# Performance work log

Measured on AMD Instinct MI355X. Metric: run time of the kernel, lower is better.

## Reference

```python
import jax, jax.numpy as jnp
import numpy as np

B, NQ, NKV = 4, 2048, 2048
D_MODEL, N_HEADS, D_K = 1024, 16, 64


def setup_inputs() -> dict:
    key = jax.random.key(0)
    ks = jax.random.split(key, 7)
    s = 1.0 / np.sqrt(D_MODEL)
    return {
        "x": jax.random.normal(ks[0], (B, NQ, D_MODEL), jnp.float32),
        "encoding": jax.random.normal(ks[1], (B, NKV, D_MODEL), jnp.float32),
        "position_bias": jax.random.normal(ks[2], (1, N_HEADS, NQ, NKV), jnp.float32),
        "Wq": jax.random.normal(ks[3], (D_MODEL, D_MODEL), jnp.float32) * s,
        "Wk": jax.random.normal(ks[4], (D_MODEL, D_MODEL), jnp.float32) * s,
        "Wv": jax.random.normal(ks[5], (D_MODEL, D_MODEL), jnp.float32) * s,
        "Wo": jax.random.normal(ks[6], (D_MODEL, D_MODEL), jnp.float32) * s,
    }


def _split_heads(t):
    b, n, _ = t.shape
    return t.reshape(b, n, N_HEADS, D_K).transpose(0, 2, 1, 3)


def reference(x, encoding, position_bias, Wq, Wk, Wv, Wo):
    # Projections (flax Dense, no bias): y = x @ kernel
    Q = _split_heads(x @ Wq)            # [B,H,NQ,Dk]
    K = _split_heads(encoding @ Wk)     # [B,H,NKV,Dk]
    V = _split_heads(encoding @ Wv)     # [B,H,NKV,Dk]
    # T5-style: NO 1/sqrt(d_k) scaling; additive position bias before softmax
    scores = jnp.einsum('bhqd,bhkd->bhqk', Q, K) + position_bias
    attn = jax.nn.softmax(scores, axis=-1)
    ctx = jnp.einsum('bhqk,bhkd->bhqd', attn, V)    # [B,H,NQ,Dk]
    ctx = ctx.transpose(0, 2, 1, 3).reshape(x.shape[0], x.shape[1], D_MODEL)
    return ctx @ Wo
```

## Files before the change

kernel.cpp:

```cpp
#include <hip/hip_runtime.h>

#define B_   4
#define NQ_  2048
#define NKV_ 2048
#define H_   16
#define DK_  64
#define DM_  1024
#define DKV_ 2048

typedef _Float16 f16x8 __attribute__((ext_vector_type(8)));
typedef _Float16 f16x4 __attribute__((ext_vector_type(4)));
typedef float    f32x4 __attribute__((ext_vector_type(4)));

__device__ __forceinline__ void gload_lds16(const void* g, void* l) {
  __builtin_amdgcn_global_load_lds(
      (const __attribute__((address_space(1))) unsigned int*)g,
      (__attribute__((address_space(3))) unsigned int*)l, 16, 0, 0);
}

__global__ __launch_bounds__(256) void cast_f16(const float* __restrict__ in,
                                                _Float16* __restrict__ out, int n4) {
  int i = blockIdx.x * 256 + threadIdx.x;
  if (i >= n4) return;
  float4 v = ((const float4*)in)[i];
  f16x4 o = {(_Float16)v.x, (_Float16)v.y, (_Float16)v.z, (_Float16)v.w};
  *(f16x4*)(out + (size_t)i * 4) = o;
}

__global__ __launch_bounds__(256) void wtrans(const float* __restrict__ W,
                                              _Float16* __restrict__ Wt) {
  __shared__ float tile[32][33];
  int bx = blockIdx.x & 31, by = blockIdx.x >> 5;
  int tx = threadIdx.x & 31, ty = threadIdx.x >> 5;
#pragma unroll
  for (int j = 0; j < 4; ++j)
    tile[ty + j * 8][tx] = W[(size_t)(by * 32 + ty + j * 8) * 1024 + bx * 32 + tx];
  __syncthreads();
#pragma unroll
  for (int j = 0; j < 4; ++j)
    Wt[(size_t)(bx * 32 + ty + j * 8) * 1024 + by * 32 + tx] = (_Float16)tile[tx][ty + j * 8];
}

template <int F32OUT>
__global__ __launch_bounds__(256, 2) void gemm_bt(const _Float16* __restrict__ A,
                                                  const _Float16* __restrict__ Bt,
                                                  void* __restrict__ Cp,
                                                  int M, int N, int K) {
  __shared__ _Float16 As[128 * 32];
  __shared__ _Float16 Bs[128 * 32];
  const int nbn = N >> 7;
  const int bm = blockIdx.x / nbn, bn = blockIdx.x % nbn;
  const int t = threadIdx.x, w = t >> 6, l = t & 63;
  const int lr = l & 15, lg = l >> 4;
  const int wr = w >> 1, wc = w & 1;
  const int m0 = bm << 7, n0 = bn << 7;

  f32x4 acc[4][4] = {};

  for (int k0 = 0; k0 < K; k0 += 32) {
#pragma unroll
    for (int p = 0; p < 2; ++p) {
      int off = p * 4096 + w * 1024 + l * 16;
      int row = off >> 6;
      int col = (off & 63) >> 1;
      gload_lds16(A  + (size_t)(m0 + row) * K + k0 + col, (char*)As + p * 4096 + w * 1024);
      gload_lds16(Bt + (size_t)(n0 + row) * K + k0 + col, (char*)Bs + p * 4096 + w * 1024);
    }
    __syncthreads();
    f16x8 af[4], bq[4];
#pragma unroll
    for (int i = 0; i < 4; ++i) {
      af[i] = *(const f16x8*)((const char*)As + (wr * 64 + i * 16 + lr) * 64 + lg * 16);
      bq[i] = *(const f16x8*)((const char*)Bs + (wc * 64 + i * 16 + lr) * 64 + lg * 16);
    }
#pragma unroll
    for (int i = 0; i < 4; ++i)
#pragma unroll
      for (int j = 0; j < 4; ++j)
        acc[i][j] = __builtin_amdgcn_mfma_f32_16x16x32_f16(af[i], bq[j], acc[i][j], 0, 0, 0);
    __syncthreads();
  }
#pragma unroll
  for (int i = 0; i < 4; ++i)
#pragma unroll
    for (int j = 0; j < 4; ++j)
#pragma unroll
      for (int r = 0; r < 4; ++r) {
        size_t row = m0 + wr * 64 + i * 16 + lg * 4 + r;
        size_t col = n0 + wc * 64 + j * 16 + lr;
        if (F32OUT) ((float*)Cp)[row * N + col] = acc[i][j][r];
        else ((_Float16*)Cp)[row * N + col] = (_Float16)acc[i][j][r];
      }
}

__global__ __launch_bounds__(256) void vtrans(const _Float16* __restrict__ KVb,
                                              _Float16* __restrict__ Vt) {
  __shared__ _Float16 tile[64][72];
  int idx = blockIdx.x;
  int kt = idx & 31, h = (idx >> 5) & 15, b = idx >> 9;
  int kv0 = kt << 6;
  int t = threadIdx.x;
#pragma unroll
  for (int p = 0; p < 2; ++p) {
    int c = t + p * 256;
    int row = c >> 3, cb = (c & 7) * 16;
    f16x8 v = *(const f16x8*)(KVb + (size_t)(b * NKV_ + kv0 + row) * DKV_ + 1024 + h * 64 + cb / 2);
    *(f16x8*)((char*)&tile[row][0] + cb) = v;
  }
  __syncthreads();
  int d = t & 63, j0 = (t >> 6) * 2;
#pragma unroll
  for (int jj = 0; jj < 2; ++jj) {
    int kvs = (j0 + jj) * 8;
    f16x8 o;
#pragma unroll
    for (int u = 0; u < 8; ++u) o[u] = tile[kvs + u][d];
    *(f16x8*)(Vt + ((size_t)((b * H_ + h) * 64 + d)) * NKV_ + kv0 + kvs) = o;
  }
}

__global__ __launch_bounds__(256, 2) void attn(const _Float16* __restrict__ Qb,
                                               const _Float16* __restrict__ KVb,
                                               const _Float16* __restrict__ Vt,
                                               const float* __restrict__ bias,
                                               _Float16* __restrict__ ctx) {
  __shared__ _Float16 Ks[64 * 64];
  __shared__ _Float16 Vs[64 * 64];
  __shared__ _Float16 Ps[4][16 * 64];
  int idx = blockIdx.x;
  int b = idx & 3, qt = (idx >> 2) & 31, h = idx >> 7;
  int t = threadIdx.x, w = t >> 6, l = t & 63, lr = l & 15, lg = l >> 4;
  int qw = (qt << 6) + (w << 4);

  const _Float16* qp = Qb + (size_t)(b * NQ_ + qw + lr) * DM_ + h * 64 + lg * 8;
  f16x8 aq0 = *(const f16x8*)qp;
  f16x8 aq1 = *(const f16x8*)(qp + 32);

  f32x4 acc[4] = {};
  float mrow[4] = {-1e30f, -1e30f, -1e30f, -1e30f};
  float lsum[4] = {0.f, 0.f, 0.f, 0.f};

  const _Float16* Kbase = KVb + (size_t)b * NKV_ * DKV_ + h * 64;
  const _Float16* Vtb = Vt + (size_t)(b * H_ + h) * 64 * NKV_;
  const float* biasb = bias + ((size_t)h * NQ_ + qw + lg * 4) * NKV_;

  for (int kv0 = 0; kv0 < NKV_; kv0 += 64) {
#pragma unroll
    for (int p = 0; p < 2; ++p) {
      int c = t + p * 256;
      int row = c >> 3, cb = (c & 7) * 16;
      f16x8 kd = *(const f16x8*)(Kbase + (size_t)(kv0 + row) * DKV_ + cb / 2);
      *(f16x8*)((char*)Ks + ((row * 128 + cb) ^ ((row & 7) << 4))) = kd;
      f16x8 vd = *(const f16x8*)(Vtb + (size_t)row * NKV_ + kv0 + cb / 2);
      *(f16x8*)((char*)Vs + ((row * 128 + cb) ^ ((row & 7) << 4))) = vd;
    }
    __syncthreads();

    float bv[4][4];
#pragma unroll
    for (int r = 0; r < 4; ++r) {
      const float* bp = biasb + (size_t)r * NKV_ + kv0 + lr;
#pragma unroll
      for (int nt = 0; nt < 4; ++nt) bv[nt][r] = bp[nt * 16];
    }

    f32x4 s[4];
#pragma unroll
    for (int nt = 0; nt < 4; ++nt) {
      int row = nt * 16 + lr;
      f16x8 kf0 = *(const f16x8*)((char*)Ks + ((row * 128 + lg * 16) ^ ((row & 7) << 4)));
      f16x8 kf1 = *(const f16x8*)((char*)Ks + ((row * 128 + 64 + lg * 16) ^ ((row & 7) << 4)));
      f32x4 z = {0.f, 0.f, 0.f, 0.f};
      z = __builtin_amdgcn_mfma_f32_16x16x32_f16(aq0, kf0, z, 0, 0, 0);
      s[nt] = __builtin_amdgcn_mfma_f32_16x16x32_f16(aq1, kf1, z, 0, 0, 0);
    }
#pragma unroll
    for (int nt = 0; nt < 4; ++nt)
#pragma unroll
      for (int r = 0; r < 4; ++r) s[nt][r] += bv[nt][r];

    float corr[4], mn[4];
#pragma unroll
    for (int r = 0; r < 4; ++r) {
      float v = fmaxf(fmaxf(s[0][r], s[1][r]), fmaxf(s[2][r], s[3][r]));
      v = fmaxf(v, __shfl_xor(v, 1));
      v = fmaxf(v, __shfl_xor(v, 2));
      v = fmaxf(v, __shfl_xor(v, 4));
      v = fmaxf(v, __shfl_xor(v, 8));
      mn[r] = fmaxf(mrow[r], v);
      corr[r] = __expf(mrow[r] - mn[r]);
      mrow[r] = mn[r];
    }
    float rs[4] = {0.f, 0.f, 0.f, 0.f};
#pragma unroll
    for (int nt = 0; nt < 4; ++nt)
#pragma unroll
      for (int r = 0; r < 4; ++r) {
        float p = __expf(s[nt][r] - mn[r]);
        s[nt][r] = p;
        rs[r] += p;
      }
#pragma unroll
    for (int r = 0; r < 4; ++r) {
      float v = rs[r];
      v += __shfl_xor(v, 1);
      v += __shfl_xor(v, 2);
      v += __shfl_xor(v, 4);
      v += __shfl_xor(v, 8);
      lsum[r] = lsum[r] * corr[r] + v;
    }
#pragma unroll
    for (int nt = 0; nt < 4; ++nt)
#pragma unroll
      for (int r = 0; r < 4; ++r) acc[nt][r] *= corr[r];

#pragma unroll
    for (int r = 0; r < 4; ++r) {
      int row = lg * 4 + r;
#pragma unroll
      for (int nt = 0; nt < 4; ++nt)
        *(_Float16*)((char*)Ps[w] + ((row * 128 + (nt * 16 + lr) * 2) ^ ((row & 7) << 4))) =
            (_Float16)s[nt][r];
    }
#pragma unroll
    for (int kk = 0; kk < 2; ++kk) {
      f16x8 pa = *(const f16x8*)((char*)Ps[w] + ((lr * 128 + kk * 64 + lg * 16) ^ ((lr & 7) << 4)));
#pragma unroll
      for (int nt = 0; nt < 4; ++nt) {
        int row = nt * 16 + lr;
        f16x8 vf = *(const f16x8*)((char*)Vs + ((row * 128 + kk * 64 + lg * 16) ^ ((row & 7) << 4)));
        acc[nt] = __builtin_amdgcn_mfma_f32_16x16x32_f16(pa, vf, acc[nt], 0, 0, 0);
      }
    }
    __syncthreads();
  }

#pragma unroll
  for (int nt = 0; nt < 4; ++nt)
#pragma unroll
    for (int r = 0; r < 4; ++r) {
      float o = acc[nt][r] / lsum[r];
      size_t q = qw + lg * 4 + r;
      ctx[((size_t)b * NQ_ + q) * DM_ + h * 64 + nt * 16 + lr] = (_Float16)o;
    }
}

extern "C" void kernel_launch(void* const* d_in, const int* in_sizes, int n_in,
                              void* d_out, int out_size, void* d_ws, size_t ws_size,
                              hipStream_t stream) {
  const float* x    = (const float*)d_in[0];
  const float* enc  = (const float*)d_in[1];
  const float* bias = (const float*)d_in[2];
  const float* Wq   = (const float*)d_in[3];
  const float* Wk   = (const float*)d_in[4];
  const float* Wv   = (const float*)d_in[5];
  const float* Wo   = (const float*)d_in[6];
  char* ws = (char*)d_ws;
  const size_t MiB = 1024 * 1024;
  _Float16* WqT   = (_Float16*)(ws + 0 * MiB);
  _Float16* WkT   = (_Float16*)(ws + 2 * MiB);
  _Float16* WvT   = (_Float16*)(ws + 4 * MiB);
  _Float16* WoT   = (_Float16*)(ws + 6 * MiB);
  _Float16* xf    = (_Float16*)(ws + 8 * MiB);
  _Float16* encf  = (_Float16*)(ws + 24 * MiB);
  _Float16* Qb    = (_Float16*)(ws + 40 * MiB);
  _Float16* KVb   = (_Float16*)(ws + 56 * MiB);
  _Float16* Vt    = (_Float16*)(ws + 88 * MiB);
  _Float16* ctxf  = (_Float16*)(ws + 104 * MiB);

  wtrans<<<1024, 256, 0, stream>>>(Wq, WqT);
  wtrans<<<1024, 256, 0, stream>>>(Wk, WkT);
  wtrans<<<1024, 256, 0, stream>>>(Wv, WvT);
  wtrans<<<1024, 256, 0, stream>>>(Wo, WoT);
  cast_f16<<<8192, 256, 0, stream>>>(x, xf, 2097152);
  cast_f16<<<8192, 256, 0, stream>>>(enc, encf, 2097152);
  gemm_bt<0><<<512, 256, 0, stream>>>(xf, WqT, Qb, 8192, 1024, 1024);
  gemm_bt<0><<<1024, 256, 0, stream>>>(encf, WkT, KVb, 8192, 2048, 1024);
  vtrans<<<2048, 256, 0, stream>>>(KVb, Vt);
  attn<<<2048, 256, 0, stream>>>(Qb, KVb, Vt, bias, ctxf);
  gemm_bt<1><<<512, 256, 0, stream>>>(ctxf, WoT, d_out, 8192, 1024, 1024);
}
```

Baseline: 409.5 us.

## Double-buffer K/V tiles and process 32 query rows per wave in attention

The attention kernel now gives each wave 32 query rows instead of 16, so each block covers 128 queries and the grid halves. K/V tiles move into double-buffered shared memory, with next-tile global loads prefetched into registers. Bias loads for the next tile are issued early to overlap with compute. This raises K/V reuse per LDS load and hides global latency, at the cost of more registers and shared memory, which may reduce occupancy.

```diff
diff --git a/kernel.cpp b/kernel.cpp
--- a/kernel.cpp
+++ b/kernel.cpp
@@ -124,125 +124,176 @@
                                                const _Float16* __restrict__ Vt,
                                                const float* __restrict__ bias,
                                                _Float16* __restrict__ ctx) {
-  __shared__ _Float16 Ks[64 * 64];
-  __shared__ _Float16 Vs[64 * 64];
-  __shared__ _Float16 Ps[4][16 * 64];
+  __shared__ _Float16 Ks[2][64 * 64];
+  __shared__ _Float16 Vs[2][64 * 64];
+  __shared__ _Float16 Ps[4][32 * 64];
   int idx = blockIdx.x;
-  int b = idx & 3, qt = (idx >> 2) & 31, h = idx >> 7;
+  int b = idx & 3, qt = (idx >> 2) & 15, h = idx >> 6;
   int t = threadIdx.x, w = t >> 6, l = t & 63, lr = l & 15, lg = l >> 4;
-  int qw = (qt << 6) + (w << 4);
-
-  const _Float16* qp = Qb + (size_t)(b * NQ_ + qw + lr) * DM_ + h * 64 + lg * 8;
-  f16x8 aq0 = *(const f16x8*)qp;
-  f16x8 aq1 = *(const f16x8*)(qp + 32);
-
-  f32x4 acc[4] = {};
-  float mrow[4] = {-1e30f, -1e30f, -1e30f, -1e30f};
-  float lsum[4] = {0.f, 0.f, 0.f, 0.f};
+  int qw = (qt << 7) + (w << 5);
+
+  f16x8 aq[2][2];
+#pragma unroll
+  for (int qe = 0; qe < 2; ++qe) {
+    const _Float16* qp = Qb + (size_t)(b * NQ_ + qw + qe * 16 + lr) * DM_ + h * 64 + lg * 8;
+    aq[qe][0] = *(const f16x8*)qp;
+    aq[qe][1] = *(const f16x8*)(qp + 32);
+  }
+
+  f32x4 acc[2][4] = {};
+  float mrow[2][4], lsum[2][4];
+#pragma unroll
+  for (int qe = 0; qe < 2; ++qe)
+#pragma unroll
+    for (int r = 0; r < 4; ++r) { mrow[qe][r] = -1e30f; lsum[qe][r] = 0.f; }
 
   const _Float16* Kbase = KVb + (size_t)b * NKV_ * DKV_ + h * 64;
-  const _Float16* Vtb = Vt + (size_t)(b * H_ + h) * 64 * NKV_;
-  const float* biasb = bias + ((size_t)h * NQ_ + qw + lg * 4) * NKV_;
-
-  for (int kv0 = 0; kv0 < NKV_; kv0 += 64) {
+  const _Float16* Vtb   = Vt + (size_t)(b * H_ + h) * 64 * NKV_;
+  const float*    biasb = bias + ((size_t)h * NQ_ + qw + lg * 4) * NKV_;
+
+  const int srow = t >> 3;
+  const int scb  = (t & 7) * 16;
+
+  f16x8 kreg[2], vreg[2];
+  float bv[2][4][4];
+
+  auto LOADKV = [&](int kv0) {
 #pragma unroll
     for (int p = 0; p < 2; ++p) {
-      int c = t + p * 256;
-      int row = c >> 3, cb = (c & 7) * 16;
-      f16x8 kd = *(const f16x8*)(Kbase + (size_t)(kv0 + row) * DKV_ + cb / 2);
-      *(f16x8*)((char*)Ks + ((row * 128 + cb) ^ ((row & 7) << 4))) = kd;
-      f16x8 vd = *(const f16x8*)(Vtb + (size_t)row * NKV_ + kv0 + cb / 2);
-      *(f16x8*)((char*)Vs + ((row * 128 + cb) ^ ((row & 7) << 4))) = vd;
-    }
-    __syncthreads();
-
-    float bv[4][4];
-#pragma unroll
-    for (int r = 0; r < 4; ++r) {
-      const float* bp = biasb + (size_t)r * NKV_ + kv0 + lr;
-#pragma unroll
-      for (int nt = 0; nt < 4; ++nt) bv[nt][r] = bp[nt * 16];
-    }
-
-    f32x4 s[4];
+      int row = srow + p * 32;
+      kreg[p] = *(const f16x8*)(Kbase + (size_t)(kv0 + row) * DKV_ + scb / 2);
+      vreg[p] = *(const f16x8*)(Vtb + (size_t)row * NKV_ + kv0 + scb / 2);
+    }
+  };
+  auto WRITEKV = [&](int buf) {
+#pragma unroll
+    for (int p = 0; p < 2; ++p) {
+      int row = srow + p * 32;
+      int off = (row * 128 + scb) ^ ((row & 7) << 4);
+      *(f16x8*)((char*)Ks[buf] + off) = kreg[p];
+      *(f16x8*)((char*)Vs[buf] + off) = vreg[p];
+    }
+  };
+  auto LOADBIAS = [&](int kv0) {
+#pragma unroll
+    for (int qe = 0; qe < 2; ++qe)
+#pragma unroll
+      for (int r = 0; r < 4; ++r) {
+        const float* bp = biasb + (size_t)(qe * 16 + r) * NKV_ + kv0 + lr;
+#pragma unroll
+        for (int nt = 0; nt < 4; ++nt) bv[qe][nt][r] = bp[nt * 16];
+      }
+  };
+
+  LOADKV(0);
+  WRITEKV(0);
+  LOADKV(64);
+  LOADBIAS(0);
+  __syncthreads();
+
+  for (int it = 0; it < 32; ++it) {
+    const int cur = it & 1;
+    const int kv0 = it << 6;
+
+    WRITEKV(cur ^ 1);
+    int kvn = kv0 + 128; if (kvn > NKV_ - 64) kvn = NKV_ - 64;
+    LOADKV(kvn);
+
+    f32x4 s[2][4];
 #pragma unroll
     for (int nt = 0; nt < 4; ++nt) {
       int row = nt * 16 + lr;
-      f16x8 kf0 = *(const f16x8*)((char*)Ks + ((row * 128 + lg * 16) ^ ((row & 7) << 4)));
-      f16x8 kf1 = *(const f16x8*)((char*)Ks + ((row * 128 + 64 + lg * 16) ^ ((row & 7) << 4)));
-      f32x4 z = {0.f, 0.f, 0.f, 0.f};
-      z = __builtin_amdgcn_mfma_f32_16x16x32_f16(aq0, kf0, z, 0, 0, 0);
-      s[nt] = __builtin_amdgcn_mfma_f32_16x16x32_f16(aq1, kf1, z, 0, 0, 0);
-    }
-#pragma unroll
-    for (int nt = 0; nt < 4; ++nt)
-#pragma unroll
-      for (int r = 0; r < 4; ++r) s[nt][r] += bv[nt][r];
-
-    float corr[4], mn[4];
-#pragma unroll
-    for (int r = 0; r < 4; ++r) {
-      float v = fmaxf(fmaxf(s[0][r], s[1][r]), fmaxf(s[2][r], s[3][r]));
-      v = fmaxf(v, __shfl_xor(v, 1));
-      v = fmaxf(v, __shfl_xor(v, 2));
-      v = fmaxf(v, __shfl_xor(v, 4));
-      v = fmaxf(v, __shfl_xor(v, 8));
-      mn[r] = fmaxf(mrow[r], v);
-      corr[r] = __expf(mrow[r] - mn[r]);
-      mrow[r] = mn[r];
-    }
-    float rs[4] = {0.f, 0.f, 0.f, 0.f};
-#pragma unroll
-    for (int nt = 0; nt < 4; ++nt)
-#pragma unroll
-      for (int r = 0; r < 4; ++r) {
-        float p = __expf(s[nt][r] - mn[r]);
-        s[nt][r] = p;
-        rs[r] += p;
-      }
-#pragma unroll
-    for (int r = 0; r < 4; ++r) {
-      float v = rs[r];
-      v += __shfl_xor(v, 1);
-      v += __shfl_xor(v, 2);
-      v += __shfl_xor(v, 4);
-      v += __shfl_xor(v, 8);
-      lsum[r] = lsum[r] * corr[r] + v;
-    }
-#pragma unroll
-    for (int nt = 0; nt < 4; ++nt)
-#pragma unroll
-      for (int r = 0; r < 4; ++r) acc[nt][r] *= corr[r];
-
-#pragma unroll
-    for (int r = 0; r < 4; ++r) {
-      int row = lg * 4 + r;
+      int sw = (row & 7) << 4;
+      f16x8 kf0 = *(const f16x8*)((char*)Ks[cur] + ((row * 128 + lg * 16) ^ sw));
+      f16x8 kf1 = *(const f16x8*)((char*)Ks[cur] + ((row * 128 + 64 + lg * 16) ^ sw));
+#pragma unroll
+      for (int qe = 0; qe < 2; ++qe) {
+        f32x4 z = {0.f, 0.f, 0.f, 0.f};
+        z = __builtin_amdgcn_mfma_f32_16x16x32_f16(aq[qe][0], kf0, z, 0, 0, 0);
+        s[qe][nt] = __builtin_amdgcn_mfma_f32_16x16x32_f16(aq[qe][1], kf1, z, 0, 0, 0);
+      }
+    }
+#pragma unroll
+    for (int qe = 0; qe < 2; ++qe)
 #pragma unroll
       for (int nt = 0; nt < 4; ++nt)
-        *(_Float16*)((char*)Ps[w] + ((row * 128 + (nt * 16 + lr) * 2) ^ ((row & 7) << 4))) =
-            (_Float16)s[nt][r];
-    }
+#pragma unroll
+        for (int r = 0; r < 4; ++r) s[qe][nt][r] += bv[qe][nt][r];
+    int kvb = kv0 + 64; if (kvb > NKV_ - 64) kvb = NKV_ - 64;
+    LOADBIAS(kvb);
+
+#pragma unroll
+    for (int qe = 0; qe < 2; ++qe)
+#pragma unroll
+      for (int r = 0; r < 4; ++r) {
+        float v = fmaxf(fmaxf(s[qe][0][r], s[qe][1][r]), fmaxf(s[qe][2][r], s[qe][3][r]));
+        v = fmaxf(v, __shfl_xor(v, 1));
+        v = fmaxf(v, __shfl_xor(v, 2));
+        v = fmaxf(v, __shfl_xor(v, 4));
+        v = fmaxf(v, __shfl_xor(v, 8));
+        float mn = fmaxf(mrow[qe][r], v);
+        float corr = __expf(mrow[qe][r] - mn);
+        mrow[qe][r] = mn;
+        float rs = 0.f;
+#pragma unroll
+        for (int nt = 0; nt < 4; ++nt) {
+          float p = __expf(s[qe][nt][r] - mn);
+          s[qe][nt][r] = p;
+          rs += p;
+        }
+        rs += __shfl_xor(rs, 1);
+        rs += __shfl_xor(rs, 2);
+        rs += __shfl_xor(rs, 4);
+        rs += __shfl_xor(rs, 8);
+        lsum[qe][r] = lsum[qe][r] * corr + rs;
+#pragma unroll
+        for (int nt = 0; nt < 4; ++nt) acc[qe][nt][r] *= corr;
+      }
+
+#pragma unroll
+    for (int qe = 0; qe < 2; ++qe)
+#pragma unroll
+      for (int r = 0; r < 4; ++r) {
+        int row = qe * 16 + lg * 4 + r;
+        int sw = (row & 7) << 4;
+#pragma unroll
+        for (int nt = 0; nt < 4; ++nt)
+          *(_Float16*)((char*)Ps[w] + ((row * 128 + (nt * 16 + lr) * 2) ^ sw)) =
+              (_Float16)s[qe][nt][r];
+      }
+
 #pragma unroll
     for (int kk = 0; kk < 2; ++kk) {
-      f16x8 pa = *(const f16x8*)((char*)Ps[w] + ((lr * 128 + kk * 64 + lg * 16) ^ ((lr & 7) << 4)));
+      f16x8 pa[2];
+#pragma unroll
+      for (int qe = 0; qe < 2; ++qe) {
+        int prow = qe * 16 + lr;
+        pa[qe] = *(const f16x8*)((char*)Ps[w] +
+                 ((prow * 128 + kk * 64 + lg * 16) ^ ((prow & 7) << 4)));
+      }
 #pragma unroll
       for (int nt = 0; nt < 4; ++nt) {
         int row = nt * 16 + lr;
-        f16x8 vf = *(const f16x8*)((char*)Vs + ((row * 128 + kk * 64 + lg * 16) ^ ((row & 7) << 4)));
-        acc[nt] = __builtin_amdgcn_mfma_f32_16x16x32_f16(pa, vf, acc[nt], 0, 0, 0);
+        f16x8 vf = *(const f16x8*)((char*)Vs[cur] +
+                 ((row * 128 + kk * 64 + lg * 16) ^ ((row & 7) << 4)));
+#pragma unroll
+        for (int qe = 0; qe < 2; ++qe)
+          acc[qe][nt] = __builtin_amdgcn_mfma_f32_16x16x32_f16(pa[qe], vf, acc[qe][nt], 0, 0, 0);
       }
     }
     __syncthreads();
   }
 
 #pragma unroll
-  for (int nt = 0; nt < 4; ++nt)
-#pragma unroll
-    for (int r = 0; r < 4; ++r) {
-      float o = acc[nt][r] / lsum[r];
-      size_t q = qw + lg * 4 + r;
-      ctx[((size_t)b * NQ_ + q) * DM_ + h * 64 + nt * 16 + lr] = (_Float16)o;
-    }
+  for (int qe = 0; qe < 2; ++qe)
+#pragma unroll
+    for (int nt = 0; nt < 4; ++nt)
+#pragma unroll
+      for (int r = 0; r < 4; ++r) {
+        float o = acc[qe][nt][r] / lsum[qe][r];
+        size_t q = qw + qe * 16 + lg * 4 + r;
+        ctx[((size_t)b * NQ_ + q) * DM_ + h * 64 + nt * 16 + lr] = (_Float16)o;
+      }
 }
 
 extern "C" void kernel_launch(void* const* d_in, const int* in_sizes, int n_in,
@@ -277,6 +328,6 @@
   gemm_bt<0><<<512, 256, 0, stream>>>(xf, WqT, Qb, 8192, 1024, 1024);
   gemm_bt<0><<<1024, 256, 0, stream>>>(encf, WkT, KVb, 8192, 2048, 1024);
   vtrans<<<2048, 256, 0, stream>>>(KVb, Vt);
-  attn<<<2048, 256, 0, stream>>>(Qb, KVb, Vt, bias, ctxf);
+  attn<<<1024, 256, 0, stream>>>(Qb, KVb, Vt, bias, ctxf);
   gemm_bt<1><<<512, 256, 0, stream>>>(ctxf, WoT, d_out, 8192, 1024, 1024);
 }
```

Measured after the change: 456.3 us. 1.11x slower.

## Register-prefetch next K/V tile and bias, use exp2 softmax with setprio

Applied to the files above, without the earlier changes.

The attention loop now loads the next K/V tile and the next position-bias block into registers while the current tile is being computed, and stores them to LDS at the top of the next iteration. This hides global-load latency behind the MFMA and softmax work. The softmax is also moved to base 2: Q is pre-scaled by log2(e) in f16 and the bias by log2(e), so exp2f can be used directly. s_setprio is raised around the MFMA sections. The cost is higher register pressure, and the Q pre-scaling adds a small f16 rounding change.

```diff
diff --git a/kernel.cpp b/kernel.cpp
--- a/kernel.cpp
+++ b/kernel.cpp
@@ -127,6 +127,7 @@
   __shared__ _Float16 Ks[64 * 64];
   __shared__ _Float16 Vs[64 * 64];
   __shared__ _Float16 Ps[4][16 * 64];
+  const float LOG2E = 1.44269504f;
   int idx = blockIdx.x;
   int b = idx & 3, qt = (idx >> 2) & 31, h = idx >> 7;
   int t = threadIdx.x, w = t >> 6, l = t & 63, lr = l & 15, lg = l >> 4;
@@ -135,51 +136,78 @@
   const _Float16* qp = Qb + (size_t)(b * NQ_ + qw + lr) * DM_ + h * 64 + lg * 8;
   f16x8 aq0 = *(const f16x8*)qp;
   f16x8 aq1 = *(const f16x8*)(qp + 32);
+#pragma unroll
+  for (int u = 0; u < 8; ++u) { aq0[u] = aq0[u] * (_Float16)LOG2E; aq1[u] = aq1[u] * (_Float16)LOG2E; }
 
   f32x4 acc[4] = {};
   float mrow[4] = {-1e30f, -1e30f, -1e30f, -1e30f};
   float lsum[4] = {0.f, 0.f, 0.f, 0.f};
 
   const _Float16* Kbase = KVb + (size_t)b * NKV_ * DKV_ + h * 64;
-  const _Float16* Vtb = Vt + (size_t)(b * H_ + h) * 64 * NKV_;
-  const float* biasb = bias + ((size_t)h * NQ_ + qw + lg * 4) * NKV_;
-
-  for (int kv0 = 0; kv0 < NKV_; kv0 += 64) {
+  const _Float16* Vtb   = Vt + (size_t)(b * H_ + h) * 64 * NKV_;
+  const float*    biasb = bias + ((size_t)h * NQ_ + qw + lg * 4) * NKV_;
+
+  const int srow = t >> 3;
+  const int scb  = (t & 7) * 16;
+
+  f16x8 kreg[2], vreg[2];
+  float bv[4][4], bvn[4][4];
+
+  auto LOADKV = [&](int kv0) {
 #pragma unroll
     for (int p = 0; p < 2; ++p) {
-      int c = t + p * 256;
-      int row = c >> 3, cb = (c & 7) * 16;
-      f16x8 kd = *(const f16x8*)(Kbase + (size_t)(kv0 + row) * DKV_ + cb / 2);
-      *(f16x8*)((char*)Ks + ((row * 128 + cb) ^ ((row & 7) << 4))) = kd;
-      f16x8 vd = *(const f16x8*)(Vtb + (size_t)row * NKV_ + kv0 + cb / 2);
-      *(f16x8*)((char*)Vs + ((row * 128 + cb) ^ ((row & 7) << 4))) = vd;
-    }
-    __syncthreads();
-
-    float bv[4][4];
+      int row = srow + p * 32;
+      kreg[p] = *(const f16x8*)(Kbase + (size_t)(kv0 + row) * DKV_ + scb / 2);
+      vreg[p] = *(const f16x8*)(Vtb + (size_t)row * NKV_ + kv0 + scb / 2);
+    }
+  };
+  auto LOADBIAS = [&](int kv0, float (&dst)[4][4]) {
 #pragma unroll
     for (int r = 0; r < 4; ++r) {
       const float* bp = biasb + (size_t)r * NKV_ + kv0 + lr;
 #pragma unroll
-      for (int nt = 0; nt < 4; ++nt) bv[nt][r] = bp[nt * 16];
-    }
+      for (int nt = 0; nt < 4; ++nt) dst[nt][r] = bp[nt * 16] * LOG2E;
+    }
+  };
+
+  LOADKV(0);
+  LOADBIAS(0, bv);
+
+  for (int it = 0; it < 32; ++it) {
+    const int kv0 = it << 6;
+
+#pragma unroll
+    for (int p = 0; p < 2; ++p) {
+      int row = srow + p * 32;
+      int off = (row * 128 + scb) ^ ((row & 7) << 4);
+      *(f16x8*)((char*)Ks + off) = kreg[p];
+      *(f16x8*)((char*)Vs + off) = vreg[p];
+    }
+    __syncthreads();
+
+    const int kvn = (it < 31) ? kv0 + 64 : kv0;
+    LOADKV(kvn);
 
     f32x4 s[4];
+    __builtin_amdgcn_s_setprio(1);
 #pragma unroll
     for (int nt = 0; nt < 4; ++nt) {
       int row = nt * 16 + lr;
-      f16x8 kf0 = *(const f16x8*)((char*)Ks + ((row * 128 + lg * 16) ^ ((row & 7) << 4)));
-      f16x8 kf1 = *(const f16x8*)((char*)Ks + ((row * 128 + 64 + lg * 16) ^ ((row & 7) << 4)));
+      int sw = (row & 7) << 4;
+      f16x8 kf0 = *(const f16x8*)((char*)Ks + ((row * 128 + lg * 16) ^ sw));
+      f16x8 kf1 = *(const f16x8*)((char*)Ks + ((row * 128 + 64 + lg * 16) ^ sw));
       f32x4 z = {0.f, 0.f, 0.f, 0.f};
       z = __builtin_amdgcn_mfma_f32_16x16x32_f16(aq0, kf0, z, 0, 0, 0);
       s[nt] = __builtin_amdgcn_mfma_f32_16x16x32_f16(aq1, kf1, z, 0, 0, 0);
     }
+    __builtin_amdgcn_s_setprio(0);
+
 #pragma unroll
     for (int nt = 0; nt < 4; ++nt)
 #pragma unroll
       for (int r = 0; r < 4; ++r) s[nt][r] += bv[nt][r];
-
-    float corr[4], mn[4];
+    LOADBIAS((it < 31) ? kv0 + 64 : kv0, bvn);
+
 #pragma unroll
     for (int r = 0; r < 4; ++r) {
       float v = fmaxf(fmaxf(s[0][r], s[1][r]), fmaxf(s[2][r], s[3][r]));
@@ -187,62 +215,67 @@
       v = fmaxf(v, __shfl_xor(v, 2));
       v = fmaxf(v, __shfl_xor(v, 4));
       v = fmaxf(v, __shfl_xor(v, 8));
-      mn[r] = fmaxf(mrow[r], v);
-      corr[r] = __expf(mrow[r] - mn[r]);
-      mrow[r] = mn[r];
-    }
-    float rs[4] = {0.f, 0.f, 0.f, 0.f};
-#pragma unroll
-    for (int nt = 0; nt < 4; ++nt)
-#pragma unroll
-      for (int r = 0; r < 4; ++r) {
-        float p = __expf(s[nt][r] - mn[r]);
+      float mn = fmaxf(mrow[r], v);
+      float corr = exp2f(mrow[r] - mn);
+      mrow[r] = mn;
+      float rs = 0.f;
+#pragma unroll
+      for (int nt = 0; nt < 4; ++nt) {
+        float p = exp2f(s[nt][r] - mn);
         s[nt][r] = p;
-        rs[r] += p;
+        rs += p;
       }
-#pragma unroll
-    for (int r = 0; r < 4; ++r) {
-      float v = rs[r];
-      v += __shfl_xor(v, 1);
-      v += __shfl_xor(v, 2);
-      v += __shfl_xor(v, 4);
-      v += __shfl_xor(v, 8);
-      lsum[r] = lsum[r] * corr[r] + v;
-    }
-#pragma unroll
-    for (int nt = 0; nt < 4; ++nt)
-#pragma unroll
-      for (int r = 0; r < 4; ++r) acc[nt][r] *= corr[r];
+      rs += __shfl_xor(rs, 1);
+      rs += __shfl_xor(rs, 2);
+      rs += __shfl_xor(rs, 4);
+      rs += __shfl_xor(rs, 8);
+      lsum[r] = lsum[r] * corr + rs;
+#pragma unroll
+      for (int nt = 0; nt < 4; ++nt) acc[nt][r] *= corr;
+    }
 
 #pragma unroll
     for (int r = 0; r < 4; ++r) {
       int row = lg * 4 + r;
+      int sw = (row & 7) << 4;
 #pragma unroll
       for (int nt = 0; nt < 4; ++nt)
-        *(_Float16*)((char*)Ps[w] + ((row * 128 + (nt * 16 + lr) * 2) ^ ((row & 7) << 4))) =
+        *(_Float16*)((char*)Ps[w] + ((row * 128 + (nt * 16 + lr) * 2) ^ sw)) =
             (_Float16)s[nt][r];
     }
+
+    __builtin_amdgcn_s_setprio(1);
 #pragma unroll
     for (int kk = 0; kk < 2; ++kk) {
-      f16x8 pa = *(const f16x8*)((char*)Ps[w] + ((lr * 128 + kk * 64 + lg * 16) ^ ((lr & 7) << 4)));
+      f16x8 pa = *(const f16x8*)((char*)Ps[w] +
+                 ((lr * 128 + kk * 64 + lg * 16) ^ ((lr & 7) << 4)));
 #pragma unroll
       for (int nt = 0; nt < 4; ++nt) {
         int row = nt * 16 + lr;
-        f16x8 vf = *(const f16x8*)((char*)Vs + ((row * 128 + kk * 64 + lg * 16) ^ ((row & 7) << 4)));
+        f16x8 vf = *(const f16x8*)((char*)Vs +
+                 ((row * 128 + kk * 64 + lg * 16) ^ ((row & 7) << 4)));
         acc[nt] = __builtin_amdgcn_mfma_f32_16x16x32_f16(pa, vf, acc[nt], 0, 0, 0);
       }
     }
+    __builtin_amdgcn_s_setprio(0);
     __syncthreads();
-  }
-
-#pragma unroll
-  for (int nt = 0; nt < 4; ++nt)
-#pragma unroll
-    for (int r = 0; r < 4; ++r) {
-      float o = acc[nt][r] / lsum[r];
+
+#pragma unroll
+    for (int nt = 0; nt < 4; ++nt)
+#pragma unroll
+      for (int r = 0; r < 4; ++r) bv[nt][r] = bvn[nt][r];
+  }
+
+#pragma unroll
+  for (int r = 0; r < 4; ++r) {
+    float inv = 1.0f / lsum[r];
+#pragma unroll
+    for (int nt = 0; nt < 4; ++nt) {
+      float o = acc[nt][r] * inv;
       size_t q = qw + lg * 4 + r;
       ctx[((size_t)b * NQ_ + q) * DM_ + h * 64 + nt * 16 + lr] = (_Float16)o;
     }
+  }
 }
 
 extern "C" void kernel_launch(void* const* d_in, const int* in_sizes, int n_in,
```

Measured after the change: 398.1 us. -2.8%, faster.
